# Kernel optimization log

Measured on AMD Instinct MI355X. Metric: run time of the kernel, lower is better.

Reference implementation:

```python
import jax, jax.numpy as jnp
import numpy as np

B, C, I, H, T = 256, 16, 64, 40, 512


def setup_inputs() -> dict:
    key = jax.random.key(0)
    ks = jax.random.split(key, 7)
    s = 1.0 / np.sqrt(H)  # PyTorch GRU/Linear init scale
    return {
        "x": jax.random.normal(ks[0], (B, C, I, T), jnp.float32),
        "W_ih": jax.random.uniform(ks[1], (C, 3 * H, I), jnp.float32, -s, s),
        "W_hh": jax.random.uniform(ks[2], (C, 3 * H, H), jnp.float32, -s, s),
        "b_ih": jax.random.uniform(ks[3], (C, 3 * H), jnp.float32, -s, s),
        "b_hh": jax.random.uniform(ks[4], (C, 3 * H), jnp.float32, -s, s),
        "W_fc": jax.random.uniform(ks[5], (C, 1, H), jnp.float32, -s, s),
        "b_fc": jax.random.uniform(ks[6], (C, 1), jnp.float32, -s, s),
    }


def reference(x, W_ih, W_hh, b_ih, b_hh, W_fc, b_fc):
    # x: [B, C, I, T] -> time-major [T, B, C, I] (module permutes to batch_first [B,T,I] per channel)
    xt = jnp.transpose(x, (3, 0, 1, 2))
    hid = W_hh.shape[-1]
    # Precompute input projections for all steps/channels at once: [T, B, C, 3H]
    gi = jnp.einsum('tbci,cgi->tbcg', xt, W_ih) + b_ih

    def step(h, gi_t):
        # h: [B, C, H]
        gh = jnp.einsum('bch,cgh->bcg', h, W_hh) + b_hh  # [B, C, 3H]
        i_r, i_z, i_n = jnp.split(gi_t, 3, axis=-1)
        h_r, h_z, h_n = jnp.split(gh, 3, axis=-1)
        r = jax.nn.sigmoid(i_r + h_r)
        z = jax.nn.sigmoid(i_z + h_z)
        n = jnp.tanh(i_n + r * h_n)
        h_new = (1.0 - z) * n + z * h
        return h_new, None

    h0 = jnp.zeros((x.shape[0], x.shape[1], hid), x.dtype)
    h_final, _ = jax.lax.scan(step, h0, gi)  # final hidden [B, C, H]

    # Channel-wise FC (H -> 1) + sigmoid: [B, C, 1]
    y = jnp.einsum('bch,coh->bco', h_final, W_fc) + b_fc
    return jax.nn.sigmoid(y)
```

## Files before the change

### kernel.cpp

```cpp
#include <hip/hip_runtime.h>

#define B_ 256
#define C_ 16
#define I_ 64
#define H_ 40
#define T_ 512
#define G_ 120

#define TT  16
#define NCH (T_ / TT)
#define NT  640

#define SX  72
#define SHB 72

typedef short bf16x8 __attribute__((ext_vector_type(8)));
typedef float f32x4  __attribute__((ext_vector_type(4)));

__device__ __forceinline__ unsigned short f2bf(float f) {
    unsigned u = __float_as_uint(f);
    unsigned r = (u + 0x7FFFu + ((u >> 16) & 1u)) >> 16;
    return (unsigned short)r;
}
__device__ __forceinline__ float bf2f(unsigned s) {
    return __uint_as_float(s << 16);
}
__device__ __forceinline__ float sigf(float x) {
    return __builtin_amdgcn_rcpf(1.0f + __expf(-x));
}

__device__ __forceinline__ void step_barrier() {
    asm volatile("s_waitcnt lgkmcnt(0)" ::: "memory");
    __builtin_amdgcn_s_barrier();
    asm volatile("" ::: "memory");
}

__global__ __launch_bounds__(NT, 1)
void gru_mfma_kernel(const float* __restrict__ x,
                     const float* __restrict__ Wih,
                     const float* __restrict__ Whh,
                     const float* __restrict__ bih,
                     const float* __restrict__ bhh,
                     const float* __restrict__ Wfc,
                     const float* __restrict__ bfc,
                     float* __restrict__ out)
{
    __shared__ __align__(16) unsigned short xa[2][256 * SX];
    __shared__ __align__(16) unsigned short hbf[2][16 * SHB];

    const int tid = threadIdx.x;
    const int c   = blockIdx.x >> 4;
    const int b0  = (blockIdx.x & 15) * 16;
    const int w   = tid >> 6;
    const int lan = tid & 63;
    const int lq  = lan >> 4;
    const int lm  = lan & 15;
    const int k   = w * 4 + lq;

    for (int idx = tid; idx < 2 * 16 * SHB; idx += NT)
        ((unsigned short*)hbf)[idx] = 0;

    float hreg = 0.0f;

    float4 pf[7];
#define PREFETCH(T0)                                                           \
    {                                                                          \
        _Pragma("unroll")                                                      \
        for (int it = 0; it < 7; ++it) {                                       \
            int idx = tid + it * NT;                                           \
            if (idx < 4096) {                                                  \
                int q = idx & 3, i = (idx >> 2) & 63, b = idx >> 8;            \
                const float* p = x + ((((size_t)(b0 + b) * C_ + c) * I_ + i)   \
                                      * T_ + (T0) + q * 4);                    \
                pf[it] = *reinterpret_cast<const float4*>(p);                  \
            }                                                                  \
        }                                                                      \
    }

#define STAGE(bufi)                                                            \
    {                                                                          \
        _Pragma("unroll")                                                      \
        for (int it = 0; it < 7; ++it) {                                       \
            int idx = tid + it * NT;                                           \
            if (idx < 4096) {                                                  \
                int q = idx & 3, i = (idx >> 2) & 63, b = idx >> 8;            \
                int colp = (((i >> 3) ^ q) << 3) | (i & 7);                    \
                float4 v = pf[it];                                             \
                unsigned short* xr = &xa[bufi][(q * 64 + b) * SX + colp];      \
                xr[0]       = f2bf(v.x);                                       \
                xr[16 * SX] = f2bf(v.y);                                       \
                xr[32 * SX] = f2bf(v.z);                                       \
                xr[48 * SX] = f2bf(v.w);                                       \
            }                                                                  \
        }                                                                      \
    }

    PREFETCH(0);

    bf16x8 wihf[2], whhf[2];
    {
        const int p  = w * 16 + lm;
        const int pg = p & 3;
        const int pk = p >> 2;
        #pragma unroll
        for (int ks = 0; ks < 2; ++ks) {
            bf16x8 a  = {0,0,0,0,0,0,0,0};
            bf16x8 hh = {0,0,0,0,0,0,0,0};
            if (pg < 3) {
                const float* wp = Wih + ((size_t)c * G_ + pg * H_ + pk) * I_ + ks * 32 + lq * 8;
                float4 v0 = *reinterpret_cast<const float4*>(wp);
                float4 v1 = *reinterpret_cast<const float4*>(wp + 4);
                a[0]=(short)f2bf(v0.x); a[1]=(short)f2bf(v0.y);
                a[2]=(short)f2bf(v0.z); a[3]=(short)f2bf(v0.w);
                a[4]=(short)f2bf(v1.x); a[5]=(short)f2bf(v1.y);
                a[6]=(short)f2bf(v1.z); a[7]=(short)f2bf(v1.w);
                if (ks == 0 || lq == 0) {
                    const float* hp = Whh + ((size_t)c * G_ + pg * H_ + pk) * H_ + ks * 32 + lq * 8;
                    float4 u0 = *reinterpret_cast<const float4*>(hp);
                    float4 u1 = *reinterpret_cast<const float4*>(hp + 4);
                    hh[0]=(short)f2bf(u0.x); hh[1]=(short)f2bf(u0.y);
                    hh[2]=(short)f2bf(u0.z); hh[3]=(short)f2bf(u0.w);
                    hh[4]=(short)f2bf(u1.x); hh[5]=(short)f2bf(u1.y);
                    hh[6]=(short)f2bf(u1.z); hh[7]=(short)f2bf(u1.w);
                }
            }
            wihf[ks] = a;
            whhf[ks] = hh;
        }
    }

    f32x4 bias4;
    #pragma unroll
    for (int r = 0; r < 4; ++r) {
        float v = 0.0f;
        if (r < 3) v  = bhh[c * G_ + r * H_ + k];
        if (r < 2) v += bih[c * G_ + r * H_ + k];
        bias4[r] = v;
    }
    const float bihn = bih[c * G_ + 2 * H_ + k];
    const float wfck = Wfc[c * H_ + k];

    uint2 gi_reg[16];

#define GI(bufi, nt)                                                             \
    {                                                                            \
        const unsigned short* xp =                                               \
            &xa[bufi][((nt) * 16 + lm) * SX + ((lq ^ ((nt) >> 2)) << 3)];        \
        bf16x8 xb0 = *reinterpret_cast<const bf16x8*>(xp);                       \
        bf16x8 xb1 = *reinterpret_cast<const bf16x8*>(xp + 32);                  \
        f32x4 acc = {0.f, 0.f, 0.f, 0.f};                                        \
        acc = __builtin_amdgcn_mfma_f32_16x16x32_bf16(wihf[0], xb0, acc, 0, 0, 0);\
        acc = __builtin_amdgcn_mfma_f32_16x16x32_bf16(wihf[1], xb1, acc, 0, 0, 0);\
        gi_reg[nt].x = (unsigned)f2bf(acc[0]) | ((unsigned)f2bf(acc[1]) << 16);  \
        gi_reg[nt].y = (unsigned)f2bf(acc[2]) | ((unsigned)f2bf(acc[3]) << 16);  \
    }

    STAGE(0);
    step_barrier();
    PREFETCH(TT);

    for (int ch = 0; ch < NCH; ++ch) {
        const int cur = ch & 1;

        GI(cur, 0);
        GI(cur, 1);

        #pragma unroll
        for (int tt = 0; tt < TT; ++tt) {
            if (tt + 2 < TT) GI(cur, tt + 2);
            if (tt == 10 && ch + 1 < NCH) STAGE(cur ^ 1);
            if (tt == 11 && ch + 2 < NCH) PREFETCH((ch + 2) * TT);

            const unsigned short* hp = &hbf[tt & 1][lm * SHB + lq * 8];
            bf16x8 h0 = *reinterpret_cast<const bf16x8*>(hp);
            bf16x8 h1 = {0,0,0,0,0,0,0,0};
            if (lq == 0)
                h1 = *reinterpret_cast<const bf16x8*>(&hbf[tt & 1][lm * SHB + 32]);
            f32x4 a1 = bias4;
            a1 = __builtin_amdgcn_mfma_f32_16x16x32_bf16(whhf[0], h0, a1, 0, 0, 0);
            f32x4 a2 = {0.f, 0.f, 0.f, 0.f};
            a2 = __builtin_amdgcn_mfma_f32_16x16x32_bf16(whhf[1], h1, a2, 0, 0, 0);
            uint2 gv = gi_reg[tt];
            float pre_r = a1[0] + a2[0] + bf2f(gv.x & 0xffffu);
            float pre_z = a1[1] + a2[1] + bf2f(gv.x >> 16);
            float h_n   = a1[2] + a2[2];
            float i_n   = bf2f(gv.y & 0xffffu) + bihn;
            float r = sigf(pre_r);
            float z = sigf(pre_z);
            float e = __expf(2.0f * (i_n + r * h_n));
            float n = 1.0f - 2.0f * __builtin_amdgcn_rcpf(e + 1.0f);
            hreg = (1.0f - z) * n + z * hreg;
            hbf[(tt & 1) ^ 1][lm * SHB + k] = f2bf(hreg);
            step_barrier();
        }
    }

    float* red = reinterpret_cast<float*>(&xa[0][0]);
    red[tid] = hreg * wfck;
    __syncthreads();
    if (tid < 16) {
        float s = bfc[c];
        #pragma unroll
        for (int kk = 0; kk < H_; ++kk) s += red[kk * 16 + tid];
        out[(b0 + tid) * C_ + c] = sigf(s);
    }
}

extern "C" void kernel_launch(void* const* d_in, const int* in_sizes, int n_in,
                              void* d_out, int out_size, void* d_ws, size_t ws_size,
                              hipStream_t stream) {
    const float* x   = (const float*)d_in[0];
    const float* Wih = (const float*)d_in[1];
    const float* Whh = (const float*)d_in[2];
    const float* bih = (const float*)d_in[3];
    const float* bhh = (const float*)d_in[4];
    const float* Wfc = (const float*)d_in[5];
    const float* bfc = (const float*)d_in[6];
    float* out = (float*)d_out;

    dim3 grid(C_ * (B_ / 16));
    dim3 block(NT);
    gru_mfma_kernel<<<grid, block, 0, stream>>>(x, Wih, Whh, bih, bhh, Wfc, bfc, out);
}
```

Before: 810.0 us.

## Shrink block to 4 waves and fuse input projection into per-step recurrent MFMA

Cuts the block from 10 waves to 4, so each wave now handles 2–3 hidden tiles instead of one. The separate precomputed input projection (GI into bf16 registers) is dropped. Instead each step accumulates W_ih·x and W_hh·h in the same MFMA chain, with the n-gate's hidden part placed in the fourth row slot. This removes the bf16 rounding of the gi values and makes the per-step barrier cheaper with fewer waves, but each wave now runs more serial MFMA and gate work on the critical recurrent path.

```diff
diff --git a/kernel.cpp b/kernel.cpp
--- a/kernel.cpp
+++ b/kernel.cpp
@@ -9,7 +9,7 @@
 
 #define TT  16
 #define NCH (T_ / TT)
-#define NT  640
+#define NT  256
 
 #define SX  72
 #define SHB 72
@@ -22,11 +22,14 @@
     unsigned r = (u + 0x7FFFu + ((u >> 16) & 1u)) >> 16;
     return (unsigned short)r;
 }
-__device__ __forceinline__ float bf2f(unsigned s) {
-    return __uint_as_float(s << 16);
-}
 __device__ __forceinline__ float sigf(float x) {
     return __builtin_amdgcn_rcpf(1.0f + __expf(-x));
+}
+__device__ __forceinline__ bf16x8 pack8(float4 a, float4 b) {
+    bf16x8 r;
+    r[0]=(short)f2bf(a.x); r[1]=(short)f2bf(a.y); r[2]=(short)f2bf(a.z); r[3]=(short)f2bf(a.w);
+    r[4]=(short)f2bf(b.x); r[5]=(short)f2bf(b.y); r[6]=(short)f2bf(b.z); r[7]=(short)f2bf(b.w);
+    return r;
 }
 
 __device__ __forceinline__ void step_barrier() {
@@ -55,154 +58,152 @@
     const int lan = tid & 63;
     const int lq  = lan >> 4;
     const int lm  = lan & 15;
-    const int k   = w * 4 + lq;
+    const int tbase = (w < 2) ? w * 3 : 6 + (w - 2) * 2;
+    const int ntile = (w < 2) ? 3 : 2;
 
     for (int idx = tid; idx < 2 * 16 * SHB; idx += NT)
         ((unsigned short*)hbf)[idx] = 0;
 
-    float hreg = 0.0f;
-
-    float4 pf[7];
+    float hr[3] = {0.f, 0.f, 0.f};
+
+    float4 pf[16];
 #define PREFETCH(T0)                                                           \
     {                                                                          \
         _Pragma("unroll")                                                      \
-        for (int it = 0; it < 7; ++it) {                                       \
+        for (int it = 0; it < 16; ++it) {                                      \
             int idx = tid + it * NT;                                           \
-            if (idx < 4096) {                                                  \
-                int q = idx & 3, i = (idx >> 2) & 63, b = idx >> 8;            \
-                const float* p = x + ((((size_t)(b0 + b) * C_ + c) * I_ + i)   \
-                                      * T_ + (T0) + q * 4);                    \
-                pf[it] = *reinterpret_cast<const float4*>(p);                  \
-            }                                                                  \
+            int q = idx & 3, i = (idx >> 2) & 63, b = idx >> 8;                \
+            const float* p = x + ((((size_t)(b0 + b) * C_ + c) * I_ + i)       \
+                                  * T_ + (T0) + q * 4);                        \
+            pf[it] = *reinterpret_cast<const float4*>(p);                      \
         }                                                                      \
     }
 
 #define STAGE(bufi)                                                            \
     {                                                                          \
         _Pragma("unroll")                                                      \
-        for (int it = 0; it < 7; ++it) {                                       \
+        for (int it = 0; it < 16; ++it) {                                      \
             int idx = tid + it * NT;                                           \
-            if (idx < 4096) {                                                  \
-                int q = idx & 3, i = (idx >> 2) & 63, b = idx >> 8;            \
-                int colp = (((i >> 3) ^ q) << 3) | (i & 7);                    \
-                float4 v = pf[it];                                             \
-                unsigned short* xr = &xa[bufi][(q * 64 + b) * SX + colp];      \
-                xr[0]       = f2bf(v.x);                                       \
-                xr[16 * SX] = f2bf(v.y);                                       \
-                xr[32 * SX] = f2bf(v.z);                                       \
-                xr[48 * SX] = f2bf(v.w);                                       \
-            }                                                                  \
+            int q = idx & 3, i = (idx >> 2) & 63, b = idx >> 8;                \
+            int colp = (((i >> 3) ^ q) << 3) | (i & 7);                        \
+            float4 v = pf[it];                                                 \
+            unsigned short* xr = &xa[bufi][(q * 64 + b) * SX + colp];          \
+            xr[0]       = f2bf(v.x);                                           \
+            xr[16 * SX] = f2bf(v.y);                                           \
+            xr[32 * SX] = f2bf(v.z);                                           \
+            xr[48 * SX] = f2bf(v.w);                                           \
         }                                                                      \
     }
 
+#define XRD(bufi, nt, d0, d1)                                                  \
+    {                                                                          \
+        const unsigned short* xp =                                             \
+            &xa[bufi][((nt) * 16 + lm) * SX + ((lq ^ ((nt) >> 2)) << 3)];      \
+        d0 = *reinterpret_cast<const bf16x8*>(xp);                             \
+        d1 = *reinterpret_cast<const bf16x8*>(xp + 32);                        \
+    }
+
     PREFETCH(0);
 
-    bf16x8 wihf[2], whhf[2];
-    {
-        const int p  = w * 16 + lm;
-        const int pg = p & 3;
-        const int pk = p >> 2;
-        #pragma unroll
-        for (int ks = 0; ks < 2; ++ks) {
-            bf16x8 a  = {0,0,0,0,0,0,0,0};
-            bf16x8 hh = {0,0,0,0,0,0,0,0};
-            if (pg < 3) {
-                const float* wp = Wih + ((size_t)c * G_ + pg * H_ + pk) * I_ + ks * 32 + lq * 8;
-                float4 v0 = *reinterpret_cast<const float4*>(wp);
-                float4 v1 = *reinterpret_cast<const float4*>(wp + 4);
-                a[0]=(short)f2bf(v0.x); a[1]=(short)f2bf(v0.y);
-                a[2]=(short)f2bf(v0.z); a[3]=(short)f2bf(v0.w);
-                a[4]=(short)f2bf(v1.x); a[5]=(short)f2bf(v1.y);
-                a[6]=(short)f2bf(v1.z); a[7]=(short)f2bf(v1.w);
-                if (ks == 0 || lq == 0) {
-                    const float* hp = Whh + ((size_t)c * G_ + pg * H_ + pk) * H_ + ks * 32 + lq * 8;
-                    float4 u0 = *reinterpret_cast<const float4*>(hp);
-                    float4 u1 = *reinterpret_cast<const float4*>(hp + 4);
-                    hh[0]=(short)f2bf(u0.x); hh[1]=(short)f2bf(u0.y);
-                    hh[2]=(short)f2bf(u0.z); hh[3]=(short)f2bf(u0.w);
-                    hh[4]=(short)f2bf(u1.x); hh[5]=(short)f2bf(u1.y);
-                    hh[6]=(short)f2bf(u1.z); hh[7]=(short)f2bf(u1.w);
+    bf16x8 wx0[3], wx1[3], wh0[3], wh1[3];
+    f32x4  bias4[3];
+    float  wfck[3];
+    #pragma unroll
+    for (int s = 0; s < 3; ++s) {
+        bf16x8 z8 = {0,0,0,0,0,0,0,0};
+        wx0[s] = z8; wx1[s] = z8; wh0[s] = z8; wh1[s] = z8;
+        bias4[s] = (f32x4){0.f, 0.f, 0.f, 0.f};
+        wfck[s] = 0.f;
+        if (s < ntile) {
+            const int tau = tbase + s;
+            const int g   = lm & 3;
+            const int pk  = tau * 4 + (lm >> 2);
+            if (g < 3) {
+                const float* wp = Wih + ((size_t)c * G_ + g * H_ + pk) * I_ + lq * 8;
+                wx0[s] = pack8(*reinterpret_cast<const float4*>(wp),
+                               *reinterpret_cast<const float4*>(wp + 4));
+                wx1[s] = pack8(*reinterpret_cast<const float4*>(wp + 32),
+                               *reinterpret_cast<const float4*>(wp + 36));
+            }
+            const int ghh = (g == 0 || g == 1) ? g : ((g == 3) ? 2 : -1);
+            if (ghh >= 0) {
+                const float* hp0 = Whh + ((size_t)c * G_ + ghh * H_ + pk) * H_ + lq * 8;
+                wh0[s] = pack8(*reinterpret_cast<const float4*>(hp0),
+                               *reinterpret_cast<const float4*>(hp0 + 4));
+                if (lq == 0) {
+                    const float* hp1 = Whh + ((size_t)c * G_ + ghh * H_ + pk) * H_ + 32;
+                    wh1[s] = pack8(*reinterpret_cast<const float4*>(hp1),
+                                   *reinterpret_cast<const float4*>(hp1 + 4));
                 }
             }
-            wihf[ks] = a;
-            whhf[ks] = hh;
+            const int k = tau * 4 + lq;
+            bias4[s][0] = bih[c * G_ + k]          + bhh[c * G_ + k];
+            bias4[s][1] = bih[c * G_ + H_ + k]     + bhh[c * G_ + H_ + k];
+            bias4[s][2] = bih[c * G_ + 2 * H_ + k];
+            bias4[s][3] = bhh[c * G_ + 2 * H_ + k];
+            wfck[s] = Wfc[c * H_ + k];
         }
-    }
-
-    f32x4 bias4;
-    #pragma unroll
-    for (int r = 0; r < 4; ++r) {
-        float v = 0.0f;
-        if (r < 3) v  = bhh[c * G_ + r * H_ + k];
-        if (r < 2) v += bih[c * G_ + r * H_ + k];
-        bias4[r] = v;
-    }
-    const float bihn = bih[c * G_ + 2 * H_ + k];
-    const float wfck = Wfc[c * H_ + k];
-
-    uint2 gi_reg[16];
-
-#define GI(bufi, nt)                                                             \
-    {                                                                            \
-        const unsigned short* xp =                                               \
-            &xa[bufi][((nt) * 16 + lm) * SX + ((lq ^ ((nt) >> 2)) << 3)];        \
-        bf16x8 xb0 = *reinterpret_cast<const bf16x8*>(xp);                       \
-        bf16x8 xb1 = *reinterpret_cast<const bf16x8*>(xp + 32);                  \
-        f32x4 acc = {0.f, 0.f, 0.f, 0.f};                                        \
-        acc = __builtin_amdgcn_mfma_f32_16x16x32_bf16(wihf[0], xb0, acc, 0, 0, 0);\
-        acc = __builtin_amdgcn_mfma_f32_16x16x32_bf16(wihf[1], xb1, acc, 0, 0, 0);\
-        gi_reg[nt].x = (unsigned)f2bf(acc[0]) | ((unsigned)f2bf(acc[1]) << 16);  \
-        gi_reg[nt].y = (unsigned)f2bf(acc[2]) | ((unsigned)f2bf(acc[3]) << 16);  \
     }
 
     STAGE(0);
     step_barrier();
     PREFETCH(TT);
+    bf16x8 xc0, xc1;
+    XRD(0, 0, xc0, xc1);
 
     for (int ch = 0; ch < NCH; ++ch) {
         const int cur = ch & 1;
-
-        GI(cur, 0);
-        GI(cur, 1);
-
         #pragma unroll
         for (int tt = 0; tt < TT; ++tt) {
-            if (tt + 2 < TT) GI(cur, tt + 2);
             if (tt == 10 && ch + 1 < NCH) STAGE(cur ^ 1);
             if (tt == 11 && ch + 2 < NCH) PREFETCH((ch + 2) * TT);
 
-            const unsigned short* hp = &hbf[tt & 1][lm * SHB + lq * 8];
-            bf16x8 h0 = *reinterpret_cast<const bf16x8*>(hp);
-            bf16x8 h1 = {0,0,0,0,0,0,0,0};
-            if (lq == 0)
-                h1 = *reinterpret_cast<const bf16x8*>(&hbf[tt & 1][lm * SHB + 32]);
-            f32x4 a1 = bias4;
-            a1 = __builtin_amdgcn_mfma_f32_16x16x32_bf16(whhf[0], h0, a1, 0, 0, 0);
-            f32x4 a2 = {0.f, 0.f, 0.f, 0.f};
-            a2 = __builtin_amdgcn_mfma_f32_16x16x32_bf16(whhf[1], h1, a2, 0, 0, 0);
-            uint2 gv = gi_reg[tt];
-            float pre_r = a1[0] + a2[0] + bf2f(gv.x & 0xffffu);
-            float pre_z = a1[1] + a2[1] + bf2f(gv.x >> 16);
-            float h_n   = a1[2] + a2[2];
-            float i_n   = bf2f(gv.y & 0xffffu) + bihn;
-            float r = sigf(pre_r);
-            float z = sigf(pre_z);
-            float e = __expf(2.0f * (i_n + r * h_n));
-            float n = 1.0f - 2.0f * __builtin_amdgcn_rcpf(e + 1.0f);
-            hreg = (1.0f - z) * n + z * hreg;
-            hbf[(tt & 1) ^ 1][lm * SHB + k] = f2bf(hreg);
+            const unsigned short* hp = &hbf[tt & 1][lm * SHB];
+            bf16x8 h0 = *reinterpret_cast<const bf16x8*>(hp + lq * 8);
+            bf16x8 h1 = *reinterpret_cast<const bf16x8*>(hp + 32 + lq * 8);
+
+            bf16x8 xn0, xn1;
+            if (tt < TT - 1) { XRD(cur, tt + 1, xn0, xn1) }
+            else             { XRD(cur ^ 1, 0, xn0, xn1) }
+
+            #pragma unroll
+            for (int s = 0; s < 3; ++s) {
+                if (s < ntile) {
+                    f32x4 aa = bias4[s];
+                    aa = __builtin_amdgcn_mfma_f32_16x16x32_bf16(wx0[s], xc0, aa, 0, 0, 0);
+                    aa = __builtin_amdgcn_mfma_f32_16x16x32_bf16(wh0[s], h0,  aa, 0, 0, 0);
+                    f32x4 bb = {0.f, 0.f, 0.f, 0.f};
+                    bb = __builtin_amdgcn_mfma_f32_16x16x32_bf16(wx1[s], xc1, bb, 0, 0, 0);
+                    bb = __builtin_amdgcn_mfma_f32_16x16x32_bf16(wh1[s], h1,  bb, 0, 0, 0);
+                    float pre_r = aa[0] + bb[0];
+                    float pre_z = aa[1] + bb[1];
+                    float i_n   = aa[2] + bb[2];
+                    float h_n   = aa[3] + bb[3];
+                    float r = sigf(pre_r);
+                    float z = sigf(pre_z);
+                    float e = __expf(2.0f * (i_n + r * h_n));
+                    float n = 1.0f - 2.0f * __builtin_amdgcn_rcpf(e + 1.0f);
+                    hr[s] = n + z * (hr[s] - n);
+                    hbf[(tt & 1) ^ 1][lm * SHB + ((tbase + s) * 4 + lq)] = f2bf(hr[s]);
+                }
+            }
+            xc0 = xn0; xc1 = xn1;
             step_barrier();
         }
     }
 
     float* red = reinterpret_cast<float*>(&xa[0][0]);
-    red[tid] = hreg * wfck;
+    float part = 0.f;
+    #pragma unroll
+    for (int s = 0; s < 3; ++s)
+        if (s < ntile) part += hr[s] * wfck[s];
+    red[tid] = part;
     __syncthreads();
     if (tid < 16) {
-        float s = bfc[c];
+        float ssum = bfc[c];
         #pragma unroll
-        for (int kk = 0; kk < H_; ++kk) s += red[kk * 16 + tid];
-        out[(b0 + tid) * C_ + c] = sigf(s);
+        for (int j = 0; j < 16; ++j) ssum += red[j * 16 + tid];
+        out[(b0 + tid) * C_ + c] = sigf(ssum);
     }
 }
 
```

After: 842.0 us. 4.0% more time.
